# Optimization experiments

Measured on AMD Instinct MI355X. Metric: run time of the kernel, lower is better.

Reference implementation:

```python
import jax, jax.numpy as jnp
import numpy as np

N = 256        # nagents
HID = 256      # hid_size
OBS = 128      # obs_size
GAT_HID = 128  # gat_hid_size
H1 = 4         # gat_num_heads (first processor)
H2 = 1         # gat_num_heads_out (second processor)
NACT = 10      # single action head
NEG = 0.2      # leaky relu negative slope


def _lin(k, fan_in, fan_out, s=0.05):
    kw, kb = jax.random.split(k)
    return (jax.random.normal(kw, (fan_in, fan_out), jnp.float32) * s,
            jax.random.normal(kb, (fan_out,), jnp.float32) * s)


def setup_inputs() -> dict:
    key = jax.random.key(0)
    ks = jax.random.split(key, 32)
    p = {}
    p['obs'] = jax.random.normal(ks[0], (1, N, OBS), jnp.float32)
    p['hidden_state'] = jax.random.normal(ks[1], (N, HID), jnp.float32)
    p['cell_state'] = jax.random.normal(ks[2], (N, HID), jnp.float32)
    p['w_obs'], p['b_obs'] = _lin(ks[3], OBS, HID)
    p['w_ih'], p['b_ih'] = _lin(ks[4], HID, 4 * HID)   # LSTMCell input->gates (i,f,g,o)
    p['w_hh'], p['b_hh'] = _lin(ks[5], HID, 4 * HID)
    p['w_me'], p['b_me'] = _lin(ks[6], HID, HID)        # message encoder
    p['w_md'], p['b_md'] = _lin(ks[7], HID, HID)        # message decoder
    # sub_scheduler_mlp1: 2*HID -> HID//2 -> HID//8 -> 2
    p['s1_w1'], p['s1_b1'] = _lin(ks[8], 2 * HID, HID // 2)
    p['s1_w2'], p['s1_b2'] = _lin(ks[9], HID // 2, HID // 8)
    p['s1_w3'], p['s1_b3'] = _lin(ks[10], HID // 8, 2)
    # sub_scheduler_mlp2 (learn_second_graph)
    p['s2_w1'], p['s2_b1'] = _lin(ks[11], 2 * HID, HID // 2)
    p['s2_w2'], p['s2_b2'] = _lin(ks[12], HID // 2, HID // 8)
    p['s2_w3'], p['s2_b3'] = _lin(ks[13], HID // 8, 2)
    # GAT1: HID -> H1*GAT_HID (concat heads)
    p['g1_w'] = jax.random.normal(ks[14], (HID, H1 * GAT_HID), jnp.float32) * 0.05
    p['g1_ai'] = jax.random.normal(ks[15], (H1, GAT_HID), jnp.float32) * 0.05
    p['g1_aj'] = jax.random.normal(ks[16], (H1, GAT_HID), jnp.float32) * 0.05
    p['g1_b'] = jax.random.normal(ks[17], (H1 * GAT_HID,), jnp.float32) * 0.05
    # GAT2: H1*GAT_HID -> HID (average over heads)
    p['g2_w'] = jax.random.normal(ks[18], (H1 * GAT_HID, H2 * HID), jnp.float32) * 0.05
    p['g2_ai'] = jax.random.normal(ks[19], (H2, HID), jnp.float32) * 0.05
    p['g2_aj'] = jax.random.normal(ks[20], (H2, HID), jnp.float32) * 0.05
    p['g2_b'] = jax.random.normal(ks[21], (HID,), jnp.float32) * 0.05
    p['w_v'], p['b_v'] = _lin(ks[22], 2 * HID, 1)
    p['w_a'], p['b_a'] = _lin(ks[23], 2 * HID, NACT)
    return p


def _sub_scheduler(h, w1, b1, w2, b2, w3, b3, mask, key):
    # pairwise concat: pair[i,j] = [h_i, h_j]  -> [n, n, 2*hid]
    n, d = h.shape
    pair = jnp.concatenate([jnp.broadcast_to(h[:, None, :], (n, n, d)),
                            jnp.broadcast_to(h[None, :, :], (n, n, d))], axis=-1)
    z = jax.nn.relu(pair @ w1 + b1)
    z = jax.nn.relu(z @ w2 + b2)
    logits = z @ w3 + b3                                # [n, n, 2]
    # gumbel-softmax (tau=1, hard=True, straight-through)
    u = jax.random.uniform(key, logits.shape, minval=1e-10, maxval=1.0)
    gumbel = -jnp.log(-jnp.log(u))
    y = jax.nn.softmax(logits + gumbel, axis=-1)
    y_hard = jax.nn.one_hot(jnp.argmax(y, axis=-1), 2, dtype=y.dtype)
    y = y_hard + y - jax.lax.stop_gradient(y)
    adj = y[..., 1] * mask * mask.T                     # mask [n,1]
    return adj


def _gat(x, adj, W, ai, aj, b, average):
    # dense-adjacency multi-head GAT, self_loop_type=1 (force self loops)
    n = x.shape[0]
    heads, of = ai.shape
    h = (x @ W).reshape(n, heads, of)                   # [n, heads, out]
    eye = jnp.eye(n, dtype=x.dtype)
    adj = adj * (1.0 - eye) + eye
    ci = jnp.einsum('nhf,hf->nh', h, ai)
    cj = jnp.einsum('nhf,hf->nh', h, aj)
    e = jax.nn.leaky_relu(ci[:, None, :] + cj[None, :, :], NEG)   # [n, n, heads]
    att = jnp.where(adj[:, :, None] > 0, e, jnp.float32(-9e15))
    att = jax.nn.softmax(att, axis=1)
    att = att * adj[:, :, None]
    out = jnp.einsum('ijh,jhf->ihf', att, h)            # aggregate over neighbors j
    out = out.mean(axis=1) if average else out.reshape(n, heads * of)
    return out + b


def reference(obs, hidden_state, cell_state, w_obs, b_obs, w_ih, b_ih, w_hh, b_hh,
              w_me, b_me, w_md, b_md,
              s1_w1, s1_b1, s1_w2, s1_b2, s1_w3, s1_b3,
              s2_w1, s2_b1, s2_w2, s2_b2, s2_w3, s2_b3,
              g1_w, g1_ai, g1_aj, g1_b, g2_w, g2_ai, g2_aj, g2_b,
              w_v, b_v, w_a, b_a):
    x = (obs @ w_obs + b_obs)[0]                        # [n, hid]
    # LSTMCell, torch gate order (i, f, g, o)
    gates = x @ w_ih + b_ih + hidden_state @ w_hh + b_hh
    i, f, g, o = jnp.split(gates, 4, axis=-1)
    c_new = jax.nn.sigmoid(f) * cell_state + jax.nn.sigmoid(i) * jnp.tanh(g)
    h_new = jax.nn.sigmoid(o) * jnp.tanh(c_new)
    mask = jnp.ones((N, 1), jnp.float32)                # all agents alive
    comm = (h_new @ w_me + b_me) * mask
    comm_ori = comm
    adj1 = _sub_scheduler(comm, s1_w1, s1_b1, s1_w2, s1_b2, s1_w3, s1_b3,
                          mask, jax.random.key(1))
    comm = jax.nn.elu(_gat(comm, adj1, g1_w, g1_ai, g1_aj, g1_b, average=False))
    adj2 = _sub_scheduler(comm_ori, s2_w1, s2_b1, s2_w2, s2_b2, s2_w3, s2_b3,
                          mask, jax.random.key(2))
    comm = _gat(comm, adj2, g2_w, g2_ai, g2_aj, g2_b, average=True)
    comm = (comm * mask) @ w_md + b_md
    value = jnp.concatenate([h_new, comm], axis=-1) @ w_v + b_v      # [n, 1]
    hc = jnp.concatenate([h_new.reshape(1, N, HID), comm.reshape(1, N, HID)], axis=-1)
    action_out = jax.nn.log_softmax(hc @ w_a + b_a, axis=-1)         # [1, n, nact]
    return action_out, value, h_new, c_new
```

## Files before the change

### kernel.cpp

```cpp
#include <hip/hip_runtime.h>
#include <stdint.h>
#include <math.h>

#define NA 256

typedef __attribute__((ext_vector_type(4))) float f32x4;
typedef __attribute__((ext_vector_type(8))) short bfrag;
typedef __attribute__((ext_vector_type(4))) float cfrag;

__device__ __forceinline__ uint32_t rotl32_(uint32_t v, int d) {
    return (v << d) | (v >> (32 - d));
}

__device__ uint32_t jax_random_bits(uint32_t key_lo, uint32_t flat) {
    uint32_t a, b;
    bool first;
    if (flat < 65536u) { a = flat; b = flat + 65536u; first = true; }
    else               { a = flat - 65536u; b = flat; first = false; }
    uint32_t ks0 = 0u, ks1 = key_lo, ks2 = 0u ^ key_lo ^ 0x1BD11BDAu;
    uint32_t x0 = a + ks0, x1 = b + ks1;
    const int r0[4] = {13, 15, 26, 6};
    const int r1[4] = {17, 29, 16, 24};
#define TF_R4(RS) { for (int rr = 0; rr < 4; ++rr) { x0 += x1; x1 = rotl32_(x1, RS[rr]); x1 ^= x0; } }
    TF_R4(r0); x0 += ks1; x1 += ks2 + 1u;
    TF_R4(r1); x0 += ks2; x1 += ks0 + 2u;
    TF_R4(r0); x0 += ks0; x1 += ks1 + 3u;
    TF_R4(r1); x0 += ks1; x1 += ks2 + 4u;
    TF_R4(r0); x0 += ks2; x1 += ks0 + 5u;
#undef TF_R4
    return first ? x0 : x1;
}

__device__ float jax_gumbel(uint32_t key_lo, uint32_t flat) {
    uint32_t bits = jax_random_bits(key_lo, flat);
    uint32_t v = (bits >> 9) | 0x3F800000u;
    float u = __uint_as_float(v) - 1.0f;
    u = u + 1e-10f;
    u = fmaxf(1e-10f, u);
    return -logf(-logf(u));
}

__device__ __forceinline__ uint32_t f2bf(float f) {
    uint32_t u = __float_as_uint(f);
    return (u + 0x7FFFu + ((u >> 16) & 1u)) >> 16;
}

__global__ __launch_bounds__(256) void k_lstm(
        const float* __restrict__ obs, const float* __restrict__ hs,
        const float* __restrict__ cs,
        const float* __restrict__ w_obs, const float* __restrict__ b_obs,
        const float* __restrict__ w_ih, const float* __restrict__ b_ih,
        const float* __restrict__ w_hh, const float* __restrict__ b_hh,
        float* __restrict__ h_out, float* __restrict__ c_out,
        float* __restrict__ ci1, float* __restrict__ cj1,
        float* __restrict__ ci2, float* __restrict__ cj2) {
    __shared__ float o_l[8][128];
    __shared__ float h_l[8][256];
    __shared__ float x_l[8][256];
    __shared__ float red[8192];
    int r0 = blockIdx.x * 8, c0 = blockIdx.y * 32, t = threadIdx.x;
    if (blockIdx.x == 0 && blockIdx.y == 0) {
        for (int idx = t; idx < 1024; idx += 256) { ci1[idx] = 0.f; cj1[idx] = 0.f; }
        ci2[t] = 0.f; cj2[t] = 0.f;
    }
    ((f32x4*)o_l)[t] = ((const f32x4*)(obs + r0 * 128))[t];
    ((f32x4*)h_l)[t] = ((const f32x4*)(hs + r0 * 256))[t];
    ((f32x4*)h_l)[t + 256] = ((const f32x4*)(hs + r0 * 256))[t + 256];
    __syncthreads();
    {
        int ks = t >> 6, q = t & 63;
        f32x4 acc[8];
#pragma unroll
        for (int r = 0; r < 8; ++r) acc[r] = (f32x4){0.f, 0.f, 0.f, 0.f};
#pragma unroll
        for (int k = ks * 32; k < ks * 32 + 32; ++k) {
            f32x4 w = *(const f32x4*)(w_obs + k * 256 + q * 4);
#pragma unroll
            for (int r = 0; r < 8; ++r) {
                float xv = o_l[r][k];
                acc[r].x += xv * w.x; acc[r].y += xv * w.y;
                acc[r].z += xv * w.z; acc[r].w += xv * w.w;
            }
        }
#pragma unroll
        for (int r = 0; r < 8; ++r)
            *(f32x4*)&red[(ks * 8 + r) * 256 + q * 4] = acc[r];
    }
    __syncthreads();
#pragma unroll
    for (int rep = 0; rep < 8; ++rep) {
        int o = t + rep * 256;
        int r = o >> 8, c = o & 255;
        float s = b_obs[c];
#pragma unroll
        for (int k2 = 0; k2 < 4; ++k2) s += red[(k2 * 8 + r) * 256 + c];
        x_l[r][c] = s;
    }
    __syncthreads();
    {
        int ks = t >> 5, cg = t & 31;
        int g = cg >> 3, qd = cg & 7;
        int col = g * 256 + c0 + qd * 4;
        const float* W = (ks < 4) ? w_ih : w_hh;
        const float* xl = (ks < 4) ? &x_l[0][0] : &h_l[0][0];
        int kb = (ks & 3) * 64;
        f32x4 acc[8];
#pragma unroll
        for (int r = 0; r < 8; ++r) acc[r] = (f32x4){0.f, 0.f, 0.f, 0.f};
#pragma unroll
        for (int kk = 0; kk < 64; ++kk) {
            int k = kb + kk;
            f32x4 w = *(const f32x4*)(W + k * 1024 + col);
#pragma unroll
            for (int r = 0; r < 8; ++r) {
                float xv = xl[r * 256 + k];
                acc[r].x += xv * w.x; acc[r].y += xv * w.y;
                acc[r].z += xv * w.z; acc[r].w += xv * w.w;
            }
        }
        __syncthreads();
#pragma unroll
        for (int r = 0; r < 8; ++r)
            *(f32x4*)&red[(ks * 8 + r) * 128 + cg * 4] = acc[r];
    }
    __syncthreads();
    {
        int r = t >> 5, hc = t & 31;
        int gc = c0 + hc;
        float gate[4];
#pragma unroll
        for (int g = 0; g < 4; ++g) {
            float s = b_ih[g * 256 + gc] + b_hh[g * 256 + gc];
#pragma unroll
            for (int ks = 0; ks < 8; ++ks) s += red[(ks * 8 + r) * 128 + g * 32 + hc];
            gate[g] = s;
        }
        float ig = 1.f / (1.f + expf(-gate[0]));
        float fg = 1.f / (1.f + expf(-gate[1]));
        float gg = tanhf(gate[2]);
        float og = 1.f / (1.f + expf(-gate[3]));
        float cn = fg * cs[(r0 + r) * 256 + gc] + ig * gg;
        float hn = og * tanhf(cn);
        h_out[(r0 + r) * 256 + gc] = hn;
        c_out[(r0 + r) * 256 + gc] = cn;
    }
}

template<int K, int R>
__device__ __forceinline__ void gemm_core(const float* __restrict__ X, int xs, int r0,
                                          const float* __restrict__ W, int ws,
                                          const float* __restrict__ bias,
                                          float* __restrict__ Y, int ys, int t,
                                          float* xr, float* red) {
    constexpr int KQ = K / 4;
#pragma unroll
    for (int q = t; q < R * KQ; q += 256) {
        int r = q / KQ, c = q % KQ;
        ((f32x4*)xr)[r * KQ + c] = ((const f32x4*)(X + (r0 + r) * xs))[c];
    }
    __syncthreads();
    constexpr int KP = K / 16;
    int qd = t & 15, ks = t >> 4;
    f32x4 acc[R];
#pragma unroll
    for (int r = 0; r < R; ++r) acc[r] = (f32x4){0.f, 0.f, 0.f, 0.f};
#pragma unroll
    for (int k = ks * KP; k < ks * KP + KP; ++k) {
        f32x4 w = *(const f32x4*)(W + k * ws + qd * 4);
#pragma unroll
        for (int r = 0; r < R; ++r) {
            float xv = xr[r * K + k];
            acc[r].x += xv * w.x; acc[r].y += xv * w.y;
            acc[r].z += xv * w.z; acc[r].w += xv * w.w;
        }
    }
#pragma unroll
    for (int r = 0; r < R; ++r)
        *(f32x4*)&red[(ks * R + r) * 64 + qd * 4] = acc[r];
    __syncthreads();
#pragma unroll
    for (int rep = 0; rep < (R * 64 + 255) / 256; ++rep) {
        int o = t + rep * 256;
        int r = o >> 6, c = o & 63;
        float s = bias ? bias[c] : 0.f;
#pragma unroll
        for (int ks2 = 0; ks2 < 16; ++ks2) s += red[(ks2 * R + r) * 64 + c];
        Y[(r0 + r) * ys + c] = s;
    }
}

__global__ __launch_bounds__(256) void k_comm(const float* __restrict__ X,
                                              const float* __restrict__ W,
                                              const float* __restrict__ bias,
                                              float* __restrict__ Y) {
    __shared__ float xr[4 * 256];
    __shared__ float red[16 * 4 * 64];
    int cb = blockIdx.y * 64;
    gemm_core<256, 4>(X, 256, blockIdx.x * 4, W + cb, 256, bias + cb,
                      Y + cb, 256, threadIdx.x, xr, red);
}

__global__ __launch_bounds__(256) void k_mgemm(const float* __restrict__ comm,
        const float* __restrict__ g1_w, const float* __restrict__ g1ai,
        const float* __restrict__ g1aj,
        const float* __restrict__ s1w1, const float* __restrict__ s1b1,
        const float* __restrict__ s2w1, const float* __restrict__ s2b1,
        float* __restrict__ h1, float* __restrict__ A1, float* __restrict__ B1,
        float* __restrict__ A2, float* __restrict__ B2,
        float* __restrict__ ci1, float* __restrict__ cj1) {
    __shared__ float xr[8 * 256];
    __shared__ float red[16 * 8 * 64];
    int y = blockIdx.y, t = threadIdx.x, r0 = blockIdx.x * 8;
    const float* W; int ws; const float* bias; float* Y; int ys;
    if (y < 8) {
        W = g1_w + y * 64; ws = 512; bias = nullptr; Y = h1 + y * 64; ys = 512;
    } else {
        int idx = y - 8;
        int sel = idx >> 2, part = (idx >> 1) & 1, half = idx & 1;
        W = (sel ? s2w1 : s1w1) + part * (256 * 128) + half * 64; ws = 128;
        bias = part ? nullptr : ((sel ? s2b1 : s1b1) + half * 64);
        float* tgt = sel ? (part ? B2 : A2) : (part ? B1 : A1);
        Y = tgt + half * 64; ys = 128;
    }
#pragma unroll
    for (int q = t; q < 512; q += 256) {
        int r = q >> 6, c = q & 63;
        ((f32x4*)xr)[r * 64 + c] = ((const f32x4*)(comm + (r0 + r) * 256))[c];
    }
    __syncthreads();
    int qd = t & 15, ks = t >> 4;
    f32x4 acc[8];
#pragma unroll
    for (int r = 0; r < 8; ++r) acc[r] = (f32x4){0.f, 0.f, 0.f, 0.f};
#pragma unroll
    for (int k = ks * 16; k < ks * 16 + 16; ++k) {
        f32x4 w = *(const f32x4*)(W + k * ws + qd * 4);
#pragma unroll
        for (int r = 0; r < 8; ++r) {
            float xv = xr[r * 256 + k];
            acc[r].x += xv * w.x; acc[r].y += xv * w.y;
            acc[r].z += xv * w.z; acc[r].w += xv * w.w;
        }
    }
#pragma unroll
    for (int r = 0; r < 8; ++r)
        *(f32x4*)&red[(ks * 8 + r) * 64 + qd * 4] = acc[r];
    __syncthreads();
#pragma unroll
    for (int rep = 0; rep < 2; ++rep) {
        int o = t + rep * 256;
        int r = o >> 6, c = o & 63;
        float s = bias ? bias[c] : 0.f;
#pragma unroll
        for (int ks2 = 0; ks2 < 16; ++ks2) s += red[(ks2 * 8 + r) * 64 + c];
        Y[(r0 + r) * ys + c] = s;
        if (y < 8) {
            int h = y >> 1;
            int f = ((y & 1) << 6) + c;
            float pi = s * g1ai[h * 128 + f];
            float pj = s * g1aj[h * 128 + f];
#pragma unroll
            for (int off = 32; off; off >>= 1) {
                pi += __shfl_xor(pi, off);
                pj += __shfl_xor(pj, off);
            }
            if ((t & 63) == 0) {
                atomicAdd(&ci1[(r0 + r) * 4 + h], pi);
                atomicAdd(&cj1[(r0 + r) * 4 + h], pj);
            }
        }
    }
}

__global__ __launch_bounds__(256) void k_sched(
        const float* __restrict__ A1, const float* __restrict__ B1,
        const float* __restrict__ s1w2, const float* __restrict__ s1b2,
        const float* __restrict__ s1w3, const float* __restrict__ s1b3,
        const float* __restrict__ A2, const float* __restrict__ B2,
        const float* __restrict__ s2w2, const float* __restrict__ s2b2,
        const float* __restrict__ s2w3, const float* __restrict__ s2b3,
        float* __restrict__ adj1, float* __restrict__ adj2) {
    __shared__ __align__(16) char z1z2[65536];
    __shared__ __align__(16) char w2l[8192];
    __shared__ float a_l[128];
    __shared__ float b2_l[32], w3_l[64], b3_l[2];
    int i = blockIdx.x, t = threadIdx.x, s = blockIdx.y;
    const float* A  = s ? A2 : A1;
    const float* B  = s ? B2 : B1;
    const float* w2 = s ? s2w2 : s1w2;
    const float* b2 = s ? s2b2 : s1b2;
    const float* w3 = s ? s2w3 : s1w3;
    const float* b3 = s ? s2b3 : s1b3;
    float* adj = s ? adj2 : adj1;
    uint32_t key_lo = (uint32_t)(s + 1);

    if (t < 32) ((f32x4*)a_l)[t] = ((const f32x4*)(A + i * 128))[t];
    if (t < 32) b2_l[t] = b2[t];
    if (t < 64) w3_l[t] = w3[t];
    if (t < 2)  b3_l[t] = b3[t];
    {
        int c = t & 31, kq = t >> 5;
        uint32_t* dst = (uint32_t*)w2l;
#pragma unroll
        for (int e = 0; e < 8; ++e) {
            int k = kq * 16 + e * 2;
            uint32_t word = f2bf(w2[k * 32 + c]) | (f2bf(w2[(k + 1) * 32 + c]) << 16);
            int byte = (c * 256 + k * 2) ^ ((c & 7) << 4);
            dst[byte >> 2] = word;
        }
    }
    __syncthreads();
#pragma unroll
    for (int rep = 0; rep < 4; ++rep) {
        int j = (t >> 2) + rep * 64;
        int kq = t & 3;
        const f32x4* bp = (const f32x4*)(B + j * 128 + kq * 32);
        uint32_t words[16];
#pragma unroll
        for (int q = 0; q < 8; ++q) {
            f32x4 bv = bp[q];
            int k = kq * 32 + q * 4;
            float z0 = fmaxf(a_l[k] + bv.x, 0.f);
            float z1v = fmaxf(a_l[k + 1] + bv.y, 0.f);
            float z2v = fmaxf(a_l[k + 2] + bv.z, 0.f);
            float z3v = fmaxf(a_l[k + 3] + bv.w, 0.f);
            words[q * 2]     = f2bf(z0) | (f2bf(z1v) << 16);
            words[q * 2 + 1] = f2bf(z2v) | (f2bf(z3v) << 16);
        }
#pragma unroll
        for (int w4 = 0; w4 < 4; ++w4) {
            int byte = (j * 256 + kq * 64 + w4 * 16) ^ ((j & 7) << 4);
            *(uint4*)(z1z2 + byte) = make_uint4(words[w4 * 4], words[w4 * 4 + 1],
                                                words[w4 * 4 + 2], words[w4 * 4 + 3]);
        }
    }
    __syncthreads();
    int w = t >> 6, l = t & 63;
    bfrag bf[2][4];
#pragma unroll
    for (int ct = 0; ct < 2; ++ct)
#pragma unroll
        for (int ks = 0; ks < 4; ++ks) {
            int col = ct * 16 + (l & 15);
            int k = ks * 32 + (l >> 4) * 8;
            int byte = (col * 256 + k * 2) ^ ((col & 7) << 4);
            bf[ct][ks] = *(bfrag*)(w2l + byte);
        }
    cfrag acc[4][2];
    cfrag zz = {0.f, 0.f, 0.f, 0.f};
#pragma unroll
    for (int rt = 0; rt < 4; ++rt) { acc[rt][0] = zz; acc[rt][1] = zz; }
#pragma unroll
    for (int rt = 0; rt < 4; ++rt) {
        int j = (w * 4 + rt) * 16 + (l & 15);
#pragma unroll
        for (int ks = 0; ks < 4; ++ks) {
            int byte = (j * 256 + (ks * 32 + (l >> 4) * 8) * 2) ^ ((j & 7) << 4);
            bfrag af = *(bfrag*)(z1z2 + byte);
            acc[rt][0] = __builtin_amdgcn_mfma_f32_16x16x32_bf16(af, bf[0][ks], acc[rt][0], 0, 0, 0);
            acc[rt][1] = __builtin_amdgcn_mfma_f32_16x16x32_bf16(af, bf[1][ks], acc[rt][1], 0, 0, 0);
        }
    }
    __syncthreads();
    float* z2 = (float*)z1z2;
#pragma unroll
    for (int rt = 0; rt < 4; ++rt)
#pragma unroll
        for (int ct = 0; ct < 2; ++ct)
#pragma unroll
            for (int r = 0; r < 4; ++r) {
                int j = (w * 4 + rt) * 16 + (l >> 4) * 4 + r;
                int c = ct * 16 + (l & 15);
                z2[j * 36 + c] = acc[rt][ct][r];
            }
    __syncthreads();
    {
        int j = t;
        float p0 = 0.f, p1 = 0.f;
#pragma unroll
        for (int c = 0; c < 32; ++c) {
            float zv = fmaxf(z2[j * 36 + c] + b2_l[c], 0.f);
            p0 += zv * w3_l[2 * c];
            p1 += zv * w3_l[2 * c + 1];
        }
        float l0 = p0 + b3_l[0], l1 = p1 + b3_l[1];
        uint32_t flat = (uint32_t)(i * 256 + j) * 2u;
        float g0 = jax_gumbel(key_lo, flat);
        float g1 = jax_gumbel(key_lo, flat + 1u);
        adj[i * 256 + j] = (l1 + g1 > l0 + g0) ? 1.0f : 0.0f;
    }
}

__global__ __launch_bounds__(256) void k_gat1(const float* __restrict__ H,
        const float* __restrict__ adj, const float* __restrict__ ci,
        const float* __restrict__ cj, const float* __restrict__ bias,
        float* __restrict__ out) {
    __shared__ float att[2][4][256];
    __shared__ float red[4][2][256];
    int i0 = blockIdx.x * 2, cb = blockIdx.y * 256, t = threadIdx.x;
#pragma unroll
    for (int r = 0; r < 2; ++r) {
        int i = i0 + r;
        float adjv = (t == i) ? 1.f : adj[i * 256 + t];
#pragma unroll
        for (int h = 0; h < 4; ++h) {
            float e = ci[i * 4 + h] + cj[t * 4 + h];
            e = e >= 0.f ? e : 0.2f * e;
            att[r][h][t] = adjv > 0.f ? e : -INFINITY;
        }
    }
    __syncthreads();
    {
        int wv = t >> 6, lane = t & 63;
        for (int p = wv; p < 8; p += 4) {
            int r = p >> 2, h = p & 3;
            float* ar = att[r][h];
            float m = -INFINITY;
            for (int j = lane; j < 256; j += 64) m = fmaxf(m, ar[j]);
            for (int off = 32; off; off >>= 1) m = fmaxf(m, __shfl_xor(m, off));
            float vals[4], sm = 0.f;
#pragma unroll
            for (int q = 0; q < 4; ++q) {
                float v = expf(ar[lane + 64 * q] - m);
                vals[q] = v; sm += v;
            }
            for (int off = 32; off; off >>= 1) sm += __shfl_xor(sm, off);
            float inv = 1.f / sm;
#pragma unroll
            for (int q = 0; q < 4; ++q) ar[lane + 64 * q] = vals[q] * inv;
        }
    }
    __syncthreads();
    {
        int q = t & 63, js = t >> 6;
        int c = cb + q * 4;
        int h = c >> 7;
        f32x4 a0 = {0.f, 0.f, 0.f, 0.f}, a1 = a0;
        const float* ar0 = att[0][h];
        const float* ar1 = att[1][h];
#pragma unroll
        for (int j = js * 64; j < js * 64 + 64; ++j) {
            f32x4 hv = *(const f32x4*)(H + j * 512 + c);
            float v0 = ar0[j], v1 = ar1[j];
            a0.x += v0 * hv.x; a0.y += v0 * hv.y; a0.z += v0 * hv.z; a0.w += v0 * hv.w;
            a1.x += v1 * hv.x; a1.y += v1 * hv.y; a1.z += v1 * hv.z; a1.w += v1 * hv.w;
        }
        *(f32x4*)&red[js][0][q * 4] = a0;
        *(f32x4*)&red[js][1][q * 4] = a1;
    }
    __syncthreads();
#pragma unroll
    for (int rep = 0; rep < 2; ++rep) {
        int o = t + rep * 256;
        int r = o >> 8, c = o & 255;
        float s = red[0][r][c] + red[1][r][c] + red[2][r][c] + red[3][r][c] + bias[cb + c];
        out[(i0 + r) * 512 + cb + c] = s > 0.f ? s : expm1f(s);
    }
}

__global__ __launch_bounds__(256) void k_g2gemm(const float* __restrict__ comm2,
        const float* __restrict__ g2w, const float* __restrict__ g2ai,
        const float* __restrict__ g2aj, float* __restrict__ h2,
        float* __restrict__ ci2, float* __restrict__ cj2) {
    __shared__ float xr[4 * 512];
    __shared__ float red[16 * 4 * 64];
    int t = threadIdx.x, r0 = blockIdx.x * 4, cb = blockIdx.y * 64;
    const float* W = g2w + cb;
#pragma unroll
    for (int q = t; q < 512; q += 256) {
        int r = q >> 7, c = q & 127;
        ((f32x4*)xr)[r * 128 + c] = ((const f32x4*)(comm2 + (r0 + r) * 512))[c];
    }
    __syncthreads();
    int qd = t & 15, ks = t >> 4;
    f32x4 acc[4];
#pragma unroll
    for (int r = 0; r < 4; ++r) acc[r] = (f32x4){0.f, 0.f, 0.f, 0.f};
#pragma unroll
    for (int k = ks * 32; k < ks * 32 + 32; ++k) {
        f32x4 w = *(const f32x4*)(W + k * 256 + qd * 4);
#pragma unroll
        for (int r = 0; r < 4; ++r) {
            float xv = xr[r * 512 + k];
            acc[r].x += xv * w.x; acc[r].y += xv * w.y;
            acc[r].z += xv * w.z; acc[r].w += xv * w.w;
        }
    }
#pragma unroll
    for (int r = 0; r < 4; ++r)
        *(f32x4*)&red[(ks * 4 + r) * 64 + qd * 4] = acc[r];
    __syncthreads();
    {
        int o = t;
        int r = o >> 6, c = o & 63;
        float s = 0.f;
#pragma unroll
        for (int ks2 = 0; ks2 < 16; ++ks2) s += red[(ks2 * 4 + r) * 64 + c];
        h2[(r0 + r) * 256 + cb + c] = s;
        float pi = s * g2ai[cb + c];
        float pj = s * g2aj[cb + c];
#pragma unroll
        for (int off = 32; off; off >>= 1) {
            pi += __shfl_xor(pi, off);
            pj += __shfl_xor(pj, off);
        }
        if ((t & 63) == 0) {
            atomicAdd(&ci2[r0 + r], pi);
            atomicAdd(&cj2[r0 + r], pj);
        }
    }
}

__global__ __launch_bounds__(256) void k_final(const float* __restrict__ H,
        const float* __restrict__ adj, const float* __restrict__ ci,
        const float* __restrict__ cj, const float* __restrict__ g2_b,
        const float* __restrict__ w_md, const float* __restrict__ b_md,
        const float* __restrict__ h_new,
        const float* __restrict__ w_v, const float* __restrict__ b_v,
        const float* __restrict__ w_a, const float* __restrict__ b_a,
        float* __restrict__ value, float* __restrict__ action) {
    __shared__ float att[256];
    __shared__ float buf[4][256];
    __shared__ float out2[256];
    __shared__ float comm3[256];
    __shared__ float hrow[256];
    __shared__ float hred[4][16];
    __shared__ float vred[4];
    int i = blockIdx.x, t = threadIdx.x;
    hrow[t] = h_new[i * 256 + t];
    {
        float adjv = (t == i) ? 1.f : adj[i * 256 + t];
        float e = ci[i] + cj[t];
        e = e >= 0.f ? e : 0.2f * e;
        att[t] = adjv > 0.f ? e : -INFINITY;
    }
    __syncthreads();
    {
        int lane = t & 63;
        float m = -INFINITY;
        for (int j = lane; j < 256; j += 64) m = fmaxf(m, att[j]);
        for (int off = 32; off; off >>= 1) m = fmaxf(m, __shfl_xor(m, off));
        float sm = 0.f;
        for (int j = lane; j < 256; j += 64) sm += expf(att[j] - m);
        for (int off = 32; off; off >>= 1) sm += __shfl_xor(sm, off);
        float inv = 1.f / sm;
        float myval = expf(att[t] - m) * inv;
        __syncthreads();
        att[t] = myval;
    }
    __syncthreads();
    {
        int q = t & 63, js = t >> 6;
        f32x4 acc = {0.f, 0.f, 0.f, 0.f};
#pragma unroll
        for (int j = js * 64; j < js * 64 + 64; ++j) {
            f32x4 hv = *(const f32x4*)(H + j * 256 + q * 4);
            float av = att[j];
            acc.x += av * hv.x; acc.y += av * hv.y; acc.z += av * hv.z; acc.w += av * hv.w;
        }
        *(f32x4*)&buf[js][q * 4] = acc;
    }
    __syncthreads();
    out2[t] = buf[0][t] + buf[1][t] + buf[2][t] + buf[3][t] + g2_b[t];
    __syncthreads();
    {
        int q = t & 63, ks = t >> 6;
        f32x4 acc = {0.f, 0.f, 0.f, 0.f};
#pragma unroll
        for (int k = ks * 64; k < ks * 64 + 64; ++k) {
            f32x4 wv = *(const f32x4*)(w_md + k * 256 + q * 4);
            float xv = out2[k];
            acc.x += xv * wv.x; acc.y += xv * wv.y; acc.z += xv * wv.z; acc.w += xv * wv.w;
        }
        *(f32x4*)&buf[ks][q * 4] = acc;
    }
    __syncthreads();
    comm3[t] = buf[0][t] + buf[1][t] + buf[2][t] + buf[3][t] + b_md[t];
    __syncthreads();
    int w = t >> 6, l = t & 63;
    {
        float p = hrow[t] * w_v[t] + comm3[t] * w_v[256 + t];
        for (int off = 32; off; off >>= 1) p += __shfl_xor(p, off);
        if (l == 0) vred[w] = p;
    }
    {
        int o = l & 15;
        int kseg = w * 4 + (l >> 4);
        float acc = 0.f;
        if (o < 10) {
#pragma unroll
            for (int kk = 0; kk < 32; ++kk) {
                int k = kseg * 32 + kk;
                float x = (kseg < 8) ? hrow[k] : comm3[k - 256];
                acc += x * w_a[k * 10 + o];
            }
        }
        acc += __shfl_xor(acc, 16);
        acc += __shfl_xor(acc, 32);
        if (l < 16) hred[w][l] = acc;
    }
    __syncthreads();
    if (t < 16) {
        int o = t;
        float logit = (o < 10)
            ? hred[0][o] + hred[1][o] + hred[2][o] + hred[3][o] + b_a[o]
            : -INFINITY;
        float m = logit;
        for (int off = 8; off; off >>= 1) m = fmaxf(m, __shfl_xor(m, off));
        float ex = (o < 10) ? expf(logit - m) : 0.f;
        float sm = ex;
        for (int off = 8; off; off >>= 1) sm += __shfl_xor(sm, off);
        if (o < 10) action[i * 10 + o] = logit - m - logf(sm);
        if (o == 0) value[i] = vred[0] + vred[1] + vred[2] + vred[3] + b_v[0];
    }
}

extern "C" void kernel_launch(void* const* d_in, const int* in_sizes, int n_in,
                              void* d_out, int out_size, void* d_ws, size_t ws_size,
                              hipStream_t stream) {
    const float* obs   = (const float*)d_in[0];
    const float* hs    = (const float*)d_in[1];
    const float* cs    = (const float*)d_in[2];
    const float* w_obs = (const float*)d_in[3];
    const float* b_obs = (const float*)d_in[4];
    const float* w_ih  = (const float*)d_in[5];
    const float* b_ih  = (const float*)d_in[6];
    const float* w_hh  = (const float*)d_in[7];
    const float* b_hh  = (const float*)d_in[8];
    const float* w_me  = (const float*)d_in[9];
    const float* b_me  = (const float*)d_in[10];
    const float* w_md  = (const float*)d_in[11];
    const float* b_md  = (const float*)d_in[12];
    const float* s1_w1 = (const float*)d_in[13];
    const float* s1_b1 = (const float*)d_in[14];
    const float* s1_w2 = (const float*)d_in[15];
    const float* s1_b2 = (const float*)d_in[16];
    const float* s1_w3 = (const float*)d_in[17];
    const float* s1_b3 = (const float*)d_in[18];
    const float* s2_w1 = (const float*)d_in[19];
    const float* s2_b1 = (const float*)d_in[20];
    const float* s2_w2 = (const float*)d_in[21];
    const float* s2_b2 = (const float*)d_in[22];
    const float* s2_w3 = (const float*)d_in[23];
    const float* s2_b3 = (const float*)d_in[24];
    const float* g1_w  = (const float*)d_in[25];
    const float* g1_ai = (const float*)d_in[26];
    const float* g1_aj = (const float*)d_in[27];
    const float* g1_b  = (const float*)d_in[28];
    const float* g2_w  = (const float*)d_in[29];
    const float* g2_ai = (const float*)d_in[30];
    const float* g2_aj = (const float*)d_in[31];
    const float* g2_b  = (const float*)d_in[32];
    const float* w_v   = (const float*)d_in[33];
    const float* b_v   = (const float*)d_in[34];
    const float* w_a   = (const float*)d_in[35];
    const float* b_a   = (const float*)d_in[36];

    float* out = (float*)d_out;
    float* action = out;
    float* value  = out + 2560;
    float* h_new  = out + 2816;
    float* c_new  = out + 68352;

    float* ws = (float*)d_ws;
    float* comm  = ws;
    float* A1    = ws + 65536;
    float* B1    = ws + 98304;
    float* A2    = ws + 131072;
    float* B2    = ws + 163840;
    float* adj1  = ws + 196608;
    float* adj2  = ws + 262144;
    float* h1    = ws + 327680;
    float* ci1   = ws + 458752;
    float* cj1   = ws + 459776;
    float* comm2 = ws + 460800;
    float* h2    = ws + 591872;
    float* ci2   = ws + 657408;
    float* cj2   = ws + 657664;

    k_lstm<<<dim3(32, 8), 256, 0, stream>>>(obs, hs, cs, w_obs, b_obs,
                                            w_ih, b_ih, w_hh, b_hh, h_new, c_new,
                                            ci1, cj1, ci2, cj2);
    k_comm<<<dim3(64, 4), 256, 0, stream>>>(h_new, w_me, b_me, comm);
    k_mgemm<<<dim3(32, 16), 256, 0, stream>>>(comm, g1_w, g1_ai, g1_aj,
                                              s1_w1, s1_b1, s2_w1, s2_b1,
                                              h1, A1, B1, A2, B2, ci1, cj1);
    k_sched<<<dim3(256, 2), 256, 0, stream>>>(A1, B1, s1_w2, s1_b2, s1_w3, s1_b3,
                                              A2, B2, s2_w2, s2_b2, s2_w3, s2_b3,
                                              adj1, adj2);
    k_gat1<<<dim3(128, 2), 256, 0, stream>>>(h1, adj1, ci1, cj1, g1_b, comm2);
    k_g2gemm<<<dim3(64, 4), 256, 0, stream>>>(comm2, g2_w, g2_ai, g2_aj, h2, ci2, cj2);
    k_final<<<NA, 256, 0, stream>>>(h2, adj2, ci2, cj2, g2_b, w_md, b_md, h_new,
                                    w_v, b_v, w_a, b_a, value, action);
}
```

Before: 67.20 us.

## Fuse GAT2 projection GEMM into GAT1 kernel with atomic split-K accumulation

Removes the separate k_g2gemm launch. Each k_gat1 block now multiplies its two freshly computed ELU output rows, covering a 256-column slice of the K dimension, by the matching rows of g2_w. It atomically adds the partial results into h2 and into the ci2/cj2 attention coefficients. h2 is zeroed inside k_sched so the atomics start from zero. This saves a kernel launch and the comm2 round trip, at the cost of float atomics (nondeterministic summation order) and each block re-reading its 256x256 slice of g2_w.

```diff
diff --git a/kernel.cpp b/kernel.cpp
--- a/kernel.cpp
+++ b/kernel.cpp
@@ -279,12 +279,14 @@
         const float* __restrict__ A2, const float* __restrict__ B2,
         const float* __restrict__ s2w2, const float* __restrict__ s2b2,
         const float* __restrict__ s2w3, const float* __restrict__ s2b3,
-        float* __restrict__ adj1, float* __restrict__ adj2) {
+        float* __restrict__ adj1, float* __restrict__ adj2,
+        float* __restrict__ h2) {
     __shared__ __align__(16) char z1z2[65536];
     __shared__ __align__(16) char w2l[8192];
     __shared__ float a_l[128];
     __shared__ float b2_l[32], w3_l[64], b3_l[2];
     int i = blockIdx.x, t = threadIdx.x, s = blockIdx.y;
+    if (t < 128) h2[(i * 2 + s) * 128 + t] = 0.f;
     const float* A  = s ? A2 : A1;
     const float* B  = s ? B2 : B1;
     const float* w2 = s ? s2w2 : s1w2;
@@ -394,7 +396,10 @@
 __global__ __launch_bounds__(256) void k_gat1(const float* __restrict__ H,
         const float* __restrict__ adj, const float* __restrict__ ci,
         const float* __restrict__ cj, const float* __restrict__ bias,
-        float* __restrict__ out) {
+        const float* __restrict__ g2w, const float* __restrict__ g2ai,
+        const float* __restrict__ g2aj,
+        float* __restrict__ out, float* __restrict__ h2,
+        float* __restrict__ ci2, float* __restrict__ cj2) {
     __shared__ float att[2][4][256];
     __shared__ float red[4][2][256];
     int i0 = blockIdx.x * 2, cb = blockIdx.y * 256, t = threadIdx.x;
@@ -449,64 +454,47 @@
         *(f32x4*)&red[js][1][q * 4] = a1;
     }
     __syncthreads();
+    float* c2 = &att[0][0][0];
 #pragma unroll
     for (int rep = 0; rep < 2; ++rep) {
         int o = t + rep * 256;
         int r = o >> 8, c = o & 255;
         float s = red[0][r][c] + red[1][r][c] + red[2][r][c] + red[3][r][c] + bias[cb + c];
-        out[(i0 + r) * 512 + cb + c] = s > 0.f ? s : expm1f(s);
-    }
-}
-
-__global__ __launch_bounds__(256) void k_g2gemm(const float* __restrict__ comm2,
-        const float* __restrict__ g2w, const float* __restrict__ g2ai,
-        const float* __restrict__ g2aj, float* __restrict__ h2,
-        float* __restrict__ ci2, float* __restrict__ cj2) {
-    __shared__ float xr[4 * 512];
-    __shared__ float red[16 * 4 * 64];
-    int t = threadIdx.x, r0 = blockIdx.x * 4, cb = blockIdx.y * 64;
-    const float* W = g2w + cb;
-#pragma unroll
-    for (int q = t; q < 512; q += 256) {
-        int r = q >> 7, c = q & 127;
-        ((f32x4*)xr)[r * 128 + c] = ((const f32x4*)(comm2 + (r0 + r) * 512))[c];
-    }
-    __syncthreads();
-    int qd = t & 15, ks = t >> 4;
-    f32x4 acc[4];
-#pragma unroll
-    for (int r = 0; r < 4; ++r) acc[r] = (f32x4){0.f, 0.f, 0.f, 0.f};
-#pragma unroll
-    for (int k = ks * 32; k < ks * 32 + 32; ++k) {
-        f32x4 w = *(const f32x4*)(W + k * 256 + qd * 4);
-#pragma unroll
-        for (int r = 0; r < 4; ++r) {
-            float xv = xr[r * 512 + k];
-            acc[r].x += xv * w.x; acc[r].y += xv * w.y;
-            acc[r].z += xv * w.z; acc[r].w += xv * w.w;
-        }
-    }
-#pragma unroll
-    for (int r = 0; r < 4; ++r)
-        *(f32x4*)&red[(ks * 4 + r) * 64 + qd * 4] = acc[r];
-    __syncthreads();
-    {
-        int o = t;
-        int r = o >> 6, c = o & 63;
-        float s = 0.f;
-#pragma unroll
-        for (int ks2 = 0; ks2 < 16; ++ks2) s += red[(ks2 * 4 + r) * 64 + c];
-        h2[(r0 + r) * 256 + cb + c] = s;
-        float pi = s * g2ai[cb + c];
-        float pj = s * g2aj[cb + c];
+        s = s > 0.f ? s : expm1f(s);
+        out[(i0 + r) * 512 + cb + c] = s;
+        c2[r * 256 + c] = s;
+    }
+    __syncthreads();
+    {
+        int q = t & 63, ks = t >> 6;
+        f32x4 a0 = {0.f, 0.f, 0.f, 0.f}, a1 = a0;
+#pragma unroll
+        for (int k = ks * 64; k < ks * 64 + 64; ++k) {
+            f32x4 w = *(const f32x4*)(g2w + (cb + k) * 256 + q * 4);
+            float v0 = c2[k], v1 = c2[256 + k];
+            a0.x += v0 * w.x; a0.y += v0 * w.y; a0.z += v0 * w.z; a0.w += v0 * w.w;
+            a1.x += v1 * w.x; a1.y += v1 * w.y; a1.z += v1 * w.z; a1.w += v1 * w.w;
+        }
+        *(f32x4*)&red[ks][0][q * 4] = a0;
+        *(f32x4*)&red[ks][1][q * 4] = a1;
+    }
+    __syncthreads();
+#pragma unroll
+    for (int rep = 0; rep < 2; ++rep) {
+        int o = t + rep * 256;
+        int r = o >> 8, c = o & 255;
+        float v = red[0][r][c] + red[1][r][c] + red[2][r][c] + red[3][r][c];
+        atomicAdd(&h2[(i0 + r) * 256 + c], v);
+        float pi = v * g2ai[c];
+        float pj = v * g2aj[c];
 #pragma unroll
         for (int off = 32; off; off >>= 1) {
             pi += __shfl_xor(pi, off);
             pj += __shfl_xor(pj, off);
         }
         if ((t & 63) == 0) {
-            atomicAdd(&ci2[r0 + r], pi);
-            atomicAdd(&cj2[r0 + r], pj);
+            atomicAdd(&ci2[i0 + r], pi);
+            atomicAdd(&cj2[i0 + r], pj);
         }
     }
 }
@@ -687,9 +675,10 @@
                                               h1, A1, B1, A2, B2, ci1, cj1);
     k_sched<<<dim3(256, 2), 256, 0, stream>>>(A1, B1, s1_w2, s1_b2, s1_w3, s1_b3,
                                               A2, B2, s2_w2, s2_b2, s2_w3, s2_b3,
-                                              adj1, adj2);
-    k_gat1<<<dim3(128, 2), 256, 0, stream>>>(h1, adj1, ci1, cj1, g1_b, comm2);
-    k_g2gemm<<<dim3(64, 4), 256, 0, stream>>>(comm2, g2_w, g2_ai, g2_aj, h2, ci2, cj2);
+                                              adj1, adj2, h2);
+    k_gat1<<<dim3(128, 2), 256, 0, stream>>>(h1, adj1, ci1, cj1, g1_b,
+                                             g2_w, g2_ai, g2_aj,
+                                             comm2, h2, ci2, cj2);
     k_final<<<NA, 256, 0, stream>>>(h2, adj2, ci2, cj2, g2_b, w_md, b_md, h_new,
                                     w_v, b_v, w_a, b_a, value, action);
 }
```

Result: slower. 70.60 us (+5.1%).
